# Performance work log

Hardware: AMD Instinct MI355X
Metric: run time of the kernel (lower is better)

Reference implementation:

```python
import jax, jax.numpy as jnp
import numpy as np

L, N, E, NODE_D, EDGE_D, H = 3, 50000, 800000, 64, 16, 128
EPS = 1e-5


def _ln(x, g, b):
    mu = jnp.mean(x, axis=-1, keepdims=True)
    var = jnp.var(x, axis=-1, keepdims=True)
    return (x - mu) * jax.lax.rsqrt(var + EPS) * g + b


def setup_inputs() -> dict:
    key = jax.random.key(0)
    ks = jax.random.split(key, 16)
    inp = {
        "x": jax.random.normal(ks[0], (N, NODE_D), dtype=jnp.float32),
        "edge_index": jax.random.randint(ks[1], (2, E), 0, N, dtype=jnp.int64 if jax.config.jax_enable_x64 else jnp.int32),
        "edge_attr": jax.random.normal(ks[2], (E, EDGE_D), dtype=jnp.float32),
        # node_embed: Linear(node_dim, H) + LayerNorm
        "node_W": jax.random.normal(ks[3], (H, NODE_D), dtype=jnp.float32) * (2.0 / H) ** 0.5,
        "node_b": jnp.zeros((H,), jnp.float32),
        "node_ln_g": jnp.ones((H,), jnp.float32),
        "node_ln_b": jnp.zeros((H,), jnp.float32),
        # per-layer GINConv params, stacked on leading layer dim
        "edge_W": jax.random.normal(ks[4], (L, H, EDGE_D), dtype=jnp.float32) * (2.0 / H) ** 0.5,
        "edge_b": jnp.zeros((L, H), jnp.float32),
        "edge_ln_g": jnp.ones((L, H), jnp.float32),
        "edge_ln_b": jnp.zeros((L, H), jnp.float32),
        "sl_attr": jax.random.normal(ks[5], (L, 1, EDGE_D), dtype=jnp.float32),
        "mlp_W1": jax.random.normal(ks[6], (L, 2 * H, H), dtype=jnp.float32) * (1.0 / H) ** 0.5,
        "mlp_b1": jnp.zeros((L, 2 * H), jnp.float32),
        "mlp_W2": jax.random.normal(ks[7], (L, H, 2 * H), dtype=jnp.float32) * (1.0 / (2 * H)) ** 0.5,
        "mlp_b2": jnp.zeros((L, H), jnp.float32),
        # BatchNorm1d affine params (batch-stat / training-mode math)
        "bn_g": jnp.ones((L, H), jnp.float32),
        "bn_b": jnp.zeros((L, H), jnp.float32),
    }
    return inp


def reference(x, edge_index, edge_attr, node_W, node_b, node_ln_g, node_ln_b,
              edge_W, edge_b, edge_ln_g, edge_ln_b, sl_attr,
              mlp_W1, mlp_b1, mlp_W2, mlp_b2, bn_g, bn_b):
    n = x.shape[0]
    # augmented edge list with self loops appended (add_self_loops)
    loop = jnp.arange(n, dtype=edge_index.dtype)
    src = jnp.concatenate([edge_index[0], loop])  # [E+N]
    dst = jnp.concatenate([edge_index[1], loop])  # [E+N]

    # node_embed: Linear -> LN -> ReLU
    h = jax.nn.relu(_ln(x @ node_W.T + node_b, node_ln_g, node_ln_b))

    for l in range(L):
        # edge_embed on [original edges ; learned self-loop attr]
        sl = jnp.broadcast_to(sl_attr[l], (n, EDGE_D))
        ea = jnp.concatenate([edge_attr, sl], axis=0)          # [E+N, edge_dim]
        ea = jax.nn.relu(_ln(ea @ edge_W[l].T + edge_b[l], edge_ln_g[l], edge_ln_b[l]))
        # message: gather x_j + edge_attr; aggregate: scatter-add to dst
        msg = h[src] + ea                                      # [E+N, H]
        aggr = jax.ops.segment_sum(msg, dst, num_segments=n)   # [N, H]
        # update MLP: Linear -> GELU -> Linear (dropout inactive at eval)
        z = jax.nn.gelu(aggr @ mlp_W1[l].T + mlp_b1[l], approximate=False)
        hl = z @ mlp_W2[l].T + mlp_b2[l]
        # BatchNorm1d (training-mode batch statistics over node dim)
        mu = jnp.mean(hl, axis=0, keepdims=True)
        var = jnp.var(hl, axis=0, keepdims=True)
        hl = (hl - mu) * jax.lax.rsqrt(var + EPS) * bn_g[l] + bn_b[l]
        if l != L - 1:
            hl = jax.nn.relu(hl)  # drop_ratio = 0 -> dropout is identity
        h = hl
    return h
```

## Files before the change

### kernel.cpp

```cpp
#include <hip/hip_runtime.h>
#include <cstdint>
#include <cstddef>

#define HD 128
#define EDGED 16
#define NODED 64
#define LN_EPS 1e-5f

typedef __bf16 bf16x8 __attribute__((ext_vector_type(8)));
typedef float  f32x4  __attribute__((ext_vector_type(4)));

__device__ __forceinline__ float gelu_exact(float x) {
    return 0.5f * x * (1.0f + erff(x * 0.7071067811865475f));
}

__global__ void wconv_k(const float* __restrict__ in, __bf16* __restrict__ hi,
                        __bf16* __restrict__ lo, int n) {
    int i = blockIdx.x * blockDim.x + threadIdx.x;
    if (i < n) {
        float v = in[i];
        __bf16 h = (__bf16)v;
        hi[i] = h;
        lo[i] = (__bf16)(v - (float)h);
    }
}


__global__ void hist_k(const int* __restrict__ ei, int* __restrict__ cnt, int E) {
    int e = blockIdx.x * blockDim.x + threadIdx.x;
    if (e < E) atomicAdd(&cnt[ei[E + e]], 1);
}

__global__ void scan1_k(const int* __restrict__ in, int* __restrict__ out,
                        int* __restrict__ bsum, int n) {
    __shared__ int lds[256];
    int t = threadIdx.x;
    int i = blockIdx.x * 256 + t;
    int v = (i < n) ? in[i] : 0;
    lds[t] = v;
    __syncthreads();
#pragma unroll
    for (int o = 1; o < 256; o <<= 1) {
        int u = (t >= o) ? lds[t - o] : 0;
        __syncthreads();
        lds[t] += u;
        __syncthreads();
    }
    if (i < n) out[i] = lds[t] - v;
    if (t == 255) bsum[blockIdx.x] = lds[255];
}

__global__ void scan2_k(const int* __restrict__ bsum, int* __restrict__ boff, int nb) {
    __shared__ int lds[256];
    int t = threadIdx.x;
    int v = (t < nb) ? bsum[t] : 0;
    lds[t] = v;
    __syncthreads();
#pragma unroll
    for (int o = 1; o < 256; o <<= 1) {
        int u = (t >= o) ? lds[t - o] : 0;
        __syncthreads();
        lds[t] += u;
        __syncthreads();
    }
    if (t < nb) boff[t] = lds[t] - v;
}

__global__ void scan3_k(int* __restrict__ rs, int* __restrict__ cursor,
                        const int* __restrict__ boff, int n, int E) {
    int i = blockIdx.x * 256 + threadIdx.x;
    if (i < n) {
        int v = rs[i] + boff[blockIdx.x];
        rs[i] = v;
        cursor[i] = v;
    }
    if (i == 0) rs[n] = E;
}

__global__ void scatter_k(const int* __restrict__ ei, int* __restrict__ cursor,
                          int2* __restrict__ es, int E) {
    int e = blockIdx.x * blockDim.x + threadIdx.x;
    if (e < E) {
        int dst = ei[E + e];
        int slot = atomicAdd(&cursor[dst], 1);
        es[slot] = make_int2(ei[e], e);
    }
}

__global__ void prep_k(const float* __restrict__ edge_W, const float* __restrict__ edge_b,
                       const float* __restrict__ edge_g, const float* __restrict__ edge_be,
                       const float* __restrict__ sl_attr, float* __restrict__ Wg3,
                       float* __restrict__ bg3, float* __restrict__ M3,
                       float* __restrict__ v3, float* __restrict__ s03,
                       float* __restrict__ slv3)
{
    const int l = blockIdx.x;
    const float* W = edge_W + (size_t)l * HD * EDGED;
    const float* b = edge_b + l * HD;
    const float* g = edge_g + l * HD;
    __shared__ float Wp[HD * EDGED];
    __shared__ float bp[HD];
    __shared__ float wm[EDGED];
    __shared__ float Msh[256];
    __shared__ float vsh[EDGED];
    __shared__ float ash[EDGED];
    __shared__ float bmS, s0sh;
    const int t = threadIdx.x;
#pragma unroll
    for (int m = 0; m < 8; ++m) Wp[m * 256 + t] = W[m * 256 + t];
    __syncthreads();
    if (t < EDGED) {
        float s = 0.f;
        for (int c = 0; c < HD; ++c) s += Wp[c * EDGED + t];
        wm[t] = s * (1.f / HD);
    } else if (t == EDGED) {
        float s = 0.f;
        for (int c = 0; c < HD; ++c) s += b[c];
        bmS = s * (1.f / HD);
    }
    __syncthreads();
    if (t < HD) bp[t] = b[t] - bmS;
    __syncthreads();
#pragma unroll
    for (int m = 0; m < 8; ++m) {
        int idx = m * 256 + t;
        int c = idx >> 4, k = idx & 15;
        float val = Wp[idx] - wm[k];
        Wp[idx] = val;
        Wg3[(size_t)l * 2048 + k * HD + c] = val * g[c];
    }
    if (t < HD) bg3[l * HD + t] = bp[t] * g[t];
    __syncthreads();
    {
        int k = t >> 4, j = t & 15;
        float s = 0.f;
        for (int c = 0; c < HD; ++c) s += Wp[c * EDGED + k] * Wp[c * EDGED + j];
        Msh[t] = s;
        M3[l * 256 + t] = s;
    }
    if (t < EDGED) {
        float s = 0.f;
        for (int c = 0; c < HD; ++c) s += Wp[c * EDGED + t] * bp[c];
        vsh[t] = 2.f * s;
        v3[l * EDGED + t] = 2.f * s;
        ash[t] = sl_attr[l * EDGED + t];
    } else if (t == EDGED) {
        float s = 0.f;
        for (int c = 0; c < HD; ++c) s += bp[c] * bp[c];
        s0sh = s;
        s03[l] = s;
    }
    __syncthreads();
    if (t < HD) {
        float q = s0sh;
#pragma unroll
        for (int k = 0; k < EDGED; ++k) {
            float tk = vsh[k];
#pragma unroll
            for (int j = 0; j < EDGED; ++j) tk = fmaf(Msh[k * 16 + j], ash[j], tk);
            q = fmaf(ash[k], tk, q);
        }
        float inv = rsqrtf(q * (1.f / HD) + LN_EPS);
        float y = 0.f;
#pragma unroll
        for (int k = 0; k < EDGED; ++k) y = fmaf(Wp[t * EDGED + k], ash[k], y);
        slv3[l * HD + t] = fmaxf(fmaf(fmaf(y, g[t], bg3[l * HD + t]), inv, edge_be[l * HD + t]), 0.f);
    }
}

__launch_bounds__(256)
__global__ void einv_k(const int2* __restrict__ es, const float* __restrict__ eattr,
                       const float* __restrict__ M3, const float* __restrict__ v3,
                       const float* __restrict__ s03, float* __restrict__ einv,
                       float* __restrict__ attr_p, int* __restrict__ srcp, int E)
{
    __shared__ float Ms[3 * 256];
    __shared__ float vs[3 * 16];
    __shared__ float s0s[4];
    const int t = threadIdx.x;
    for (int i = t; i < 768; i += 256) Ms[i] = M3[i];
    if (t < 48) vs[t] = v3[t];
    if (t < 3) s0s[t] = s03[t];
    __syncthreads();
    int slot = blockIdx.x * 256 + t;
    if (slot >= E) return;
    int2 se = es[slot];
    srcp[slot] = se.x;
    const float4* ap = (const float4*)(eattr + (size_t)se.y * EDGED);
    float4 A0 = ap[0], A1 = ap[1], A2 = ap[2], A3 = ap[3];
    float4* op = (float4*)(attr_p + (size_t)slot * EDGED);
    op[0] = A0; op[1] = A1; op[2] = A2; op[3] = A3;
    float a[16] = {A0.x, A0.y, A0.z, A0.w, A1.x, A1.y, A1.z, A1.w,
                   A2.x, A2.y, A2.z, A2.w, A3.x, A3.y, A3.z, A3.w};
#pragma unroll
    for (int l = 0; l < 3; ++l) {
        float q = s0s[l];
#pragma unroll
        for (int k = 0; k < 16; ++k) {
            const float* Mr = &Ms[l * 256 + k * 16];
            float tk = vs[l * 16 + k];
#pragma unroll
            for (int j = 0; j < 16; ++j) tk = fmaf(Mr[j], a[j], tk);
            q = fmaf(a[k], tk, q);
        }
        einv[(size_t)l * E + slot] = rsqrtf(q * (1.f / HD) + LN_EPS);
    }
}

template<int K, int NC, int ACT, int STATS, int OUTBF>
__launch_bounds__(256)
__global__ void mgemm_k(const __bf16* __restrict__ Ahi, const __bf16* __restrict__ Alo,
                        const __bf16* __restrict__ Whi, const __bf16* __restrict__ Wlo,
                        const float* __restrict__ bias, float* __restrict__ C,
                        __bf16* __restrict__ Chi, __bf16* __restrict__ Clo,
                        int M, float* __restrict__ stats)
{
    constexpr int RG = 2;
    constexpr int NT = 4;
    constexpr int NK = K / 32;
    __shared__ float st_lds[2][64];

    const int t    = threadIdx.x;
    const int lane = t & 63;
    const int wv   = t >> 6;
    const int ln15 = lane & 15;
    const int quad = lane >> 4;
    const int row_base = blockIdx.x * 128 + wv * 32;
    const int col0 = blockIdx.y * 64;

    f32x4 acc[RG][NT];
#pragma unroll
    for (int g = 0; g < RG; ++g)
#pragma unroll
        for (int nt = 0; nt < NT; ++nt)
#pragma unroll
            for (int r = 0; r < 4; ++r) acc[g][nt][r] = 0.f;

    size_t arow[RG];
#pragma unroll
    for (int g = 0; g < RG; ++g) {
        int row = row_base + g * 16 + ln15;
        row = row < M ? row : M - 1;
        arow[g] = (size_t)row * K + quad * 8;
    }
    size_t brow[NT];
#pragma unroll
    for (int nt = 0; nt < NT; ++nt)
        brow[nt] = (size_t)(col0 + nt * 16 + ln15) * K + quad * 8;

    bf16x8 a0h[RG], a0l[RG], a1h[RG], a1l[RG];
    bf16x8 b0h[NT], b0l[NT], b1h[NT], b1l[NT];

#define LD_A(kc, AH, AL) { \
    _Pragma("unroll") \
    for (int g = 0; g < RG; ++g) { \
        AH[g] = *(const bf16x8*)(Ahi + arow[g] + (kc)); \
        AL[g] = *(const bf16x8*)(Alo + arow[g] + (kc)); \
    } }
#define LD_B(kc, BH, BL) { \
    _Pragma("unroll") \
    for (int nt = 0; nt < NT; ++nt) { \
        BH[nt] = *(const bf16x8*)(Whi + brow[nt] + (kc)); \
        BL[nt] = *(const bf16x8*)(Wlo + brow[nt] + (kc)); \
    } }
#define DO_MFMA(AH, AL, BH, BL) { \
    _Pragma("unroll") \
    for (int nt = 0; nt < NT; ++nt) { \
        _Pragma("unroll") \
        for (int g = 0; g < RG; ++g) { \
            acc[g][nt] = __builtin_amdgcn_mfma_f32_16x16x32_bf16(AH[g], BH[nt], acc[g][nt], 0, 0, 0); \
            acc[g][nt] = __builtin_amdgcn_mfma_f32_16x16x32_bf16(AH[g], BL[nt], acc[g][nt], 0, 0, 0); \
            acc[g][nt] = __builtin_amdgcn_mfma_f32_16x16x32_bf16(AL[g], BH[nt], acc[g][nt], 0, 0, 0); \
        } } }

    LD_A(0, a0h, a0l);
    LD_B(0, b0h, b0l);
    for (int s = 0; s < NK; s += 2) {
        LD_A((s + 1) * 32, a1h, a1l);
        LD_B((s + 1) * 32, b1h, b1l);
        DO_MFMA(a0h, a0l, b0h, b0l);
        if (s + 2 < NK) {
            LD_A((s + 2) * 32, a0h, a0l);
            LD_B((s + 2) * 32, b0h, b0l);
        }
        DO_MFMA(a1h, a1l, b1h, b1l);
    }
#undef LD_A
#undef LD_B
#undef DO_MFMA

    if (STATS) {
        if (t < 64) { st_lds[0][t] = 0.f; st_lds[1][t] = 0.f; }
        __syncthreads();
    }

    float bv[NT];
#pragma unroll
    for (int nt = 0; nt < NT; ++nt) bv[nt] = bias[col0 + nt * 16 + ln15];

    float s1[NT], s2[NT];
#pragma unroll
    for (int nt = 0; nt < NT; ++nt) { s1[nt] = 0.f; s2[nt] = 0.f; }

#pragma unroll
    for (int g = 0; g < RG; ++g)
#pragma unroll
        for (int r = 0; r < 4; ++r) {
            int row = row_base + g * 16 + quad * 4 + r;
            if (row < M) {
#pragma unroll
                for (int nt = 0; nt < NT; ++nt) {
                    float v = acc[g][nt][r] + bv[nt];
                    if (ACT == 1) v = gelu_exact(v);
                    size_t ci = (size_t)row * NC + col0 + nt * 16 + ln15;
                    if (OUTBF) {
                        __bf16 hh = (__bf16)v;
                        Chi[ci] = hh;
                        Clo[ci] = (__bf16)(v - (float)hh);
                    } else {
                        C[ci] = v;
                    }
                    if (STATS) { s1[nt] += v; s2[nt] += v * v; }
                }
            }
        }

    if (STATS) {
#pragma unroll
        for (int nt = 0; nt < NT; ++nt) {
            atomicAdd(&st_lds[0][nt * 16 + ln15], s1[nt]);
            atomicAdd(&st_lds[1][nt * 16 + ln15], s2[nt]);
        }
        __syncthreads();
        if (t < 64) {
            atomicAdd(&stats[col0 + t],      st_lds[0][t]);
            atomicAdd(&stats[HD + col0 + t], st_lds[1][t]);
        }
    }
}

__global__ void ln_relu_k(const float* __restrict__ y, const float* __restrict__ gam,
                          const float* __restrict__ bet, float* __restrict__ h, int N)
{
    int lane = threadIdx.x & 63;
    int c0 = lane * 2;
    float2 g2 = *(const float2*)&gam[c0];
    float2 b2 = *(const float2*)&bet[c0];
    int wid = (blockIdx.x * blockDim.x + threadIdx.x) >> 6;
    int nw  = (gridDim.x * blockDim.x) >> 6;
    for (int n = wid; n < N; n += nw) {
        float2 v = *(const float2*)&y[(size_t)n * HD + c0];
        float s = v.x + v.y;
        float q = v.x * v.x + v.y * v.y;
#pragma unroll
        for (int o = 32; o > 0; o >>= 1) { s += __shfl_xor(s, o, 64); q += __shfl_xor(q, o, 64); }
        float mu  = s * (1.f / 128.f);
        float inv = rsqrtf(q * (1.f / 128.f) - mu * mu + LN_EPS);
        float2 r;
        r.x = fmaxf(fmaf((v.x - mu) * inv, g2.x, b2.x), 0.f);
        r.y = fmaxf(fmaf((v.y - mu) * inv, g2.y, b2.y), 0.f);
        *(float2*)&h[(size_t)n * HD + c0] = r;
    }
}

__launch_bounds__(256)
__global__ void pull4_k(const float* __restrict__ h, const int* __restrict__ srcp,
                        const int* __restrict__ rs, const float* __restrict__ attr_p,
                        const float* __restrict__ einv, const float* __restrict__ slv,
                        const float* __restrict__ Wg, const float* __restrict__ bg,
                        const float* __restrict__ bet, __bf16* __restrict__ Ahi,
                        __bf16* __restrict__ Alo, int N)
{
    __shared__ float alds_all[4][64 * EDGED];
    const int t = threadIdx.x;
    const int lane = t & 63;
    const int wv = t >> 6;
    float* alds = alds_all[wv];

    const int c0 = lane * 2;
    float w0[16], w1[16];
#pragma unroll
    for (int k = 0; k < 16; ++k) {
        float2 wp = *(const float2*)&Wg[k * HD + c0];
        w0[k] = wp.x; w1[k] = wp.y;
    }
    const float2 bgv = *(const float2*)&bg[c0];
    const float2 btv = *(const float2*)&bet[c0];

    const int n = (blockIdx.x << 2) + wv;
    if (n >= N) return;

    const float2 hself = *(const float2*)&h[(size_t)n * HD + c0];
    const float2 slvv  = *(const float2*)&slv[c0];
    float acc0 = hself.x + slvv.x;
    float acc1 = hself.y + slvv.y;

    const int beg = rs[n], end = rs[n + 1];
    for (int s0 = beg; s0 < end; s0 += 64) {
        int m = end - s0; if (m > 64) m = 64;
        int   srcv = 0;
        float ivv  = 0.f;
        if (lane < m) { srcv = srcp[s0 + lane]; ivv = einv[s0 + lane]; }
        const float4* src4 = (const float4*)(attr_p + (size_t)s0 * EDGED);
#pragma unroll
        for (int it = 0; it < 4; ++it) {
            int idx = (it << 6) + lane;
            if (idx < (m << 2)) *(float4*)&alds[idx << 2] = src4[idx];
        }
        asm volatile("s_waitcnt lgkmcnt(0)" ::: "memory");

#define EDGE_BODY(JJ, IVJ, HVJ) { \
            const float* ar = &alds[(JJ) * EDGED]; \
            float4 A0 = *(const float4*)ar,       A1 = *(const float4*)(ar + 4); \
            float4 A2 = *(const float4*)(ar + 8), A3 = *(const float4*)(ar + 12); \
            float a[16] = {A0.x, A0.y, A0.z, A0.w, A1.x, A1.y, A1.z, A1.w, \
                           A2.x, A2.y, A2.z, A2.w, A3.x, A3.y, A3.z, A3.w}; \
            float p0 = bgv.x, q0 = 0.f, p1 = bgv.y, q1 = 0.f; \
            _Pragma("unroll") \
            for (int k = 0; k < 16; k += 2) { \
                p0 = fmaf(a[k],     w0[k],     p0); \
                q0 = fmaf(a[k + 1], w0[k + 1], q0); \
                p1 = fmaf(a[k],     w1[k],     p1); \
                q1 = fmaf(a[k + 1], w1[k + 1], q1); \
            } \
            acc0 += fmaxf(fmaf(p0 + q0, IVJ, btv.x), 0.f) + HVJ.x; \
            acc1 += fmaxf(fmaf(p1 + q1, IVJ, btv.y), 0.f) + HVJ.y; \
        }

        int j = 0;
        for (; j + 4 <= m; j += 4) {
            int s_0 = __shfl(srcv, j,     64);
            int s_1 = __shfl(srcv, j + 1, 64);
            int s_2 = __shfl(srcv, j + 2, 64);
            int s_3 = __shfl(srcv, j + 3, 64);
            float i0 = __shfl(ivv, j,     64);
            float i1 = __shfl(ivv, j + 1, 64);
            float i2 = __shfl(ivv, j + 2, 64);
            float i3 = __shfl(ivv, j + 3, 64);
            float2 h0 = *(const float2*)&h[(size_t)s_0 * HD + c0];
            float2 h1 = *(const float2*)&h[(size_t)s_1 * HD + c0];
            float2 h2 = *(const float2*)&h[(size_t)s_2 * HD + c0];
            float2 h3 = *(const float2*)&h[(size_t)s_3 * HD + c0];
            EDGE_BODY(j,     i0, h0);
            EDGE_BODY(j + 1, i1, h1);
            EDGE_BODY(j + 2, i2, h2);
            EDGE_BODY(j + 3, i3, h3);
        }
        for (; j < m; ++j) {
            int s_  = __shfl(srcv, j, 64);
            float ij = __shfl(ivv, j, 64);
            float2 hj = *(const float2*)&h[(size_t)s_ * HD + c0];
            EDGE_BODY(j, ij, hj);
        }
#undef EDGE_BODY
    }
    __bf16 b0 = (__bf16)acc0, b1 = (__bf16)acc1;
    union { __bf16 b[2]; unsigned u; } ph, pl;
    ph.b[0] = b0;
    ph.b[1] = b1;
    pl.b[0] = (__bf16)(acc0 - (float)b0);
    pl.b[1] = (__bf16)(acc1 - (float)b1);
    *(unsigned*)&Ahi[(size_t)n * HD + c0] = ph.u;
    *(unsigned*)&Alo[(size_t)n * HD + c0] = pl.u;
}

__global__ void bn_k(const float* __restrict__ hl, const float* __restrict__ stats,
                     const float* __restrict__ gam, const float* __restrict__ bet,
                     float* __restrict__ out, int total4, float invN, int relu)
{
    int idx = blockIdx.x * blockDim.x + threadIdx.x;
    if (idx < total4) {
        int c4 = idx & 31;
        float4 x  = ((const float4*)hl)[idx];
        float4 s1 = ((const float4*)stats)[c4];
        float4 s2 = ((const float4*)stats)[32 + c4];
        float4 g  = ((const float4*)gam)[c4];
        float4 b  = ((const float4*)bet)[c4];
        float4 r;
        {
            float m = s1.x * invN; float v = s2.x * invN - m * m;
            r.x = fmaf((x.x - m) * rsqrtf(v + LN_EPS), g.x, b.x);
        }
        {
            float m = s1.y * invN; float v = s2.y * invN - m * m;
            r.y = fmaf((x.y - m) * rsqrtf(v + LN_EPS), g.y, b.y);
        }
        {
            float m = s1.z * invN; float v = s2.z * invN - m * m;
            r.z = fmaf((x.z - m) * rsqrtf(v + LN_EPS), g.z, b.z);
        }
        {
            float m = s1.w * invN; float v = s2.w * invN - m * m;
            r.w = fmaf((x.w - m) * rsqrtf(v + LN_EPS), g.w, b.w);
        }
        if (relu) {
            r.x = fmaxf(r.x, 0.f); r.y = fmaxf(r.y, 0.f);
            r.z = fmaxf(r.z, 0.f); r.w = fmaxf(r.w, 0.f);
        }
        ((float4*)out)[idx] = r;
    }
}

extern "C" void kernel_launch(void* const* d_in, const int* in_sizes, int n_in,
                              void* d_out, int out_size, void* d_ws, size_t ws_size,
                              hipStream_t stream)
{
    const float* x       = (const float*)d_in[0];
    const int*   ei      = (const int*)d_in[1];
    const float* eattr   = (const float*)d_in[2];
    const float* node_W  = (const float*)d_in[3];
    const float* node_b  = (const float*)d_in[4];
    const float* node_g  = (const float*)d_in[5];
    const float* node_be = (const float*)d_in[6];
    const float* edge_W  = (const float*)d_in[7];
    const float* edge_b  = (const float*)d_in[8];
    const float* edge_g  = (const float*)d_in[9];
    const float* edge_be = (const float*)d_in[10];
    const float* sl_attr = (const float*)d_in[11];
    const float* W1      = (const float*)d_in[12];
    const float* b1      = (const float*)d_in[13];
    const float* W2      = (const float*)d_in[14];
    const float* b2      = (const float*)d_in[15];
    const float* bn_g    = (const float*)d_in[16];
    const float* bn_b    = (const float*)d_in[17];

    const int N = in_sizes[0] / NODED;
    const int E = in_sizes[1] / 2;

    char* base = (char*)d_ws;
    size_t off = 0;
    auto take = [&](size_t nbytes) -> void* {
        void* p = base + off;
        off = (off + nbytes + 15) & ~(size_t)15;
        return p;
    };
    float*  h      = (float*)take((size_t)N * HD * 4);
    float*  z      = (float*)take((size_t)N * HD * 4);
    __bf16* aghi   = (__bf16*)take((size_t)N * HD * 2);
    __bf16* aglo   = (__bf16*)take((size_t)N * HD * 2);
    __bf16* zhi    = (__bf16*)take((size_t)N * 256 * 2);
    __bf16* zlo    = (__bf16*)take((size_t)N * 256 * 2);
    __bf16* xhi    = (__bf16*)take((size_t)N * NODED * 2);
    __bf16* xlo    = (__bf16*)take((size_t)N * NODED * 2);
    float*  slv3   = (float*)take(3 * HD * 4);
    float*  stats  = (float*)take(3 * 256 * 4);
    int*    cnt    = (int*)take((size_t)N * 4);
    int*    cursor = (int*)take((size_t)N * 4);
    int*    bsum   = (int*)take(256 * 4);
    int*    boff   = (int*)take(256 * 4);
    int*    rs     = (int*)take(((size_t)N + 2) * 4);
    int2*   es     = (int2*)take((size_t)E * 8);
    float*  einv   = (float*)take((size_t)3 * E * 4);
    float*  attr_p = (float*)take((size_t)E * EDGED * 4);
    int*    srcp   = (int*)take((size_t)E * 4);
    float*  Wg3    = (float*)take(3 * 2048 * 4);
    float*  bg3    = (float*)take(3 * HD * 4);
    float*  M3     = (float*)take(3 * 256 * 4);
    float*  v3     = (float*)take(3 * 16 * 4);
    float*  s03    = (float*)take(4 * 4);
    __bf16* nWhi   = (__bf16*)take((size_t)HD * NODED * 2);
    __bf16* nWlo   = (__bf16*)take((size_t)HD * NODED * 2);
    __bf16* W1hi   = (__bf16*)take((size_t)3 * 256 * HD * 2);
    __bf16* W1lo   = (__bf16*)take((size_t)3 * 256 * HD * 2);
    __bf16* W2hi   = (__bf16*)take((size_t)3 * HD * 256 * 2);
    __bf16* W2lo   = (__bf16*)take((size_t)3 * HD * 256 * 2);

    wconv_k<<<(HD * NODED + 255) / 256, 256, 0, stream>>>(node_W, nWhi, nWlo, HD * NODED);
    wconv_k<<<(3 * 256 * HD + 255) / 256, 256, 0, stream>>>(W1, W1hi, W1lo, 3 * 256 * HD);
    wconv_k<<<(3 * 256 * HD + 255) / 256, 256, 0, stream>>>(W2, W2hi, W2lo, 3 * 256 * HD);
    wconv_k<<<((int)((size_t)N * NODED + 255) / 256), 256, 0, stream>>>(x, xhi, xlo, N * NODED);

    prep_k<<<3, 256, 0, stream>>>(edge_W, edge_b, edge_g, edge_be, sl_attr,
                                  Wg3, bg3, M3, v3, s03, slv3);

    const int eblocks = (E + 255) / 256;
    const int nblocks = (N + 255) / 256;
    hipMemsetAsync(cnt, 0, (size_t)N * sizeof(int), stream);
    hist_k<<<eblocks, 256, 0, stream>>>(ei, cnt, E);
    scan1_k<<<nblocks, 256, 0, stream>>>(cnt, rs, bsum, N);
    scan2_k<<<1, 256, 0, stream>>>(bsum, boff, nblocks);
    scan3_k<<<nblocks, 256, 0, stream>>>(rs, cursor, boff, N, E);
    scatter_k<<<eblocks, 256, 0, stream>>>(ei, cursor, es, E);

    einv_k<<<eblocks, 256, 0, stream>>>(es, eattr, M3, v3, s03, einv, attr_p, srcp, E);

    const int total4  = N * (HD / 4);
    const int vblocks = (total4 + 255) / 256;
    const int pblocks = (N + 3) / 4;
    const int gb128   = (N + 127) / 128;

    mgemm_k<NODED, HD, 0, 0, 0><<<dim3(gb128, 2), 256, 0, stream>>>(
        xhi, xlo, nWhi, nWlo, node_b, z, nullptr, nullptr, N, nullptr);
    ln_relu_k<<<pblocks, 256, 0, stream>>>(z, node_g, node_be, h, N);

    hipMemsetAsync(stats, 0, 3 * 256 * sizeof(float), stream);

    for (int l = 0; l < 3; ++l) {
        pull4_k<<<pblocks, 256, 0, stream>>>(h, srcp, rs, attr_p,
                                             einv + (size_t)l * E,
                                             slv3 + l * HD, Wg3 + (size_t)l * 2048,
                                             bg3 + l * HD, edge_be + l * HD,
                                             aghi, aglo, N);

        mgemm_k<HD, 256, 1, 0, 1><<<dim3(gb128, 4), 256, 0, stream>>>(
            aghi, aglo, W1hi + (size_t)l * 256 * HD, W1lo + (size_t)l * 256 * HD,
            b1 + l * 256, nullptr, zhi, zlo, N, nullptr);

        mgemm_k<256, HD, 0, 1, 0><<<dim3(gb128, 2), 256, 0, stream>>>(
            zhi, zlo, W2hi + (size_t)l * HD * 256, W2lo + (size_t)l * HD * 256,
            b2 + l * HD, (float*)d_out, nullptr, nullptr, N, stats + l * 256);

        bn_k<<<vblocks, 256, 0, stream>>>((const float*)d_out, stats + l * 256,
                                          bn_g + l * HD, bn_b + l * HD,
                                          (l < 2) ? h : (float*)d_out, total4, 1.f / N, (l < 2) ? 1 : 0);
    }
}
```

Before: 999.0 us.

## Store node features in fp16 and use persistent grid-stride pull kernel

Node hidden state h is now stored as fp16 instead of fp32. ln_relu_k and bn_k write it that way and pull5_k reads it, which halves the bytes of the random gathers over edges. The pull kernel also becomes a persistent grid-stride loop capped at 2048 blocks, so per-block setup such as weight register loads is paid less often. The cost is lower precision in the gathered features.

```diff
diff --git a/kernel.cpp b/kernel.cpp
--- a/kernel.cpp
+++ b/kernel.cpp
@@ -9,6 +9,8 @@
 
 typedef __bf16 bf16x8 __attribute__((ext_vector_type(8)));
 typedef float  f32x4  __attribute__((ext_vector_type(4)));
+typedef _Float16 half2v __attribute__((ext_vector_type(2)));
+typedef _Float16 half4v __attribute__((ext_vector_type(4)));
 
 __device__ __forceinline__ float gelu_exact(float x) {
     return 0.5f * x * (1.0f + erff(x * 0.7071067811865475f));
@@ -340,7 +342,7 @@
 }
 
 __global__ void ln_relu_k(const float* __restrict__ y, const float* __restrict__ gam,
-                          const float* __restrict__ bet, float* __restrict__ h, int N)
+                          const float* __restrict__ bet, _Float16* __restrict__ h16, int N)
 {
     int lane = threadIdx.x & 63;
     int c0 = lane * 2;
@@ -356,15 +358,15 @@
         for (int o = 32; o > 0; o >>= 1) { s += __shfl_xor(s, o, 64); q += __shfl_xor(q, o, 64); }
         float mu  = s * (1.f / 128.f);
         float inv = rsqrtf(q * (1.f / 128.f) - mu * mu + LN_EPS);
-        float2 r;
-        r.x = fmaxf(fmaf((v.x - mu) * inv, g2.x, b2.x), 0.f);
-        r.y = fmaxf(fmaf((v.y - mu) * inv, g2.y, b2.y), 0.f);
-        *(float2*)&h[(size_t)n * HD + c0] = r;
+        half2v r;
+        r.x = (_Float16)fmaxf(fmaf((v.x - mu) * inv, g2.x, b2.x), 0.f);
+        r.y = (_Float16)fmaxf(fmaf((v.y - mu) * inv, g2.y, b2.y), 0.f);
+        *(half2v*)&h16[(size_t)n * HD + c0] = r;
     }
 }
 
 __launch_bounds__(256)
-__global__ void pull4_k(const float* __restrict__ h, const int* __restrict__ srcp,
+__global__ void pull5_k(const _Float16* __restrict__ h16, const int* __restrict__ srcp,
                         const int* __restrict__ rs, const float* __restrict__ attr_p,
                         const float* __restrict__ einv, const float* __restrict__ slv,
                         const float* __restrict__ Wg, const float* __restrict__ bg,
@@ -384,30 +386,29 @@
         float2 wp = *(const float2*)&Wg[k * HD + c0];
         w0[k] = wp.x; w1[k] = wp.y;
     }
-    const float2 bgv = *(const float2*)&bg[c0];
-    const float2 btv = *(const float2*)&bet[c0];
-
-    const int n = (blockIdx.x << 2) + wv;
-    if (n >= N) return;
-
-    const float2 hself = *(const float2*)&h[(size_t)n * HD + c0];
-    const float2 slvv  = *(const float2*)&slv[c0];
-    float acc0 = hself.x + slvv.x;
-    float acc1 = hself.y + slvv.y;
-
-    const int beg = rs[n], end = rs[n + 1];
-    for (int s0 = beg; s0 < end; s0 += 64) {
-        int m = end - s0; if (m > 64) m = 64;
-        int   srcv = 0;
-        float ivv  = 0.f;
-        if (lane < m) { srcv = srcp[s0 + lane]; ivv = einv[s0 + lane]; }
-        const float4* src4 = (const float4*)(attr_p + (size_t)s0 * EDGED);
-#pragma unroll
-        for (int it = 0; it < 4; ++it) {
-            int idx = (it << 6) + lane;
-            if (idx < (m << 2)) *(float4*)&alds[idx << 2] = src4[idx];
-        }
-        asm volatile("s_waitcnt lgkmcnt(0)" ::: "memory");
+    const float2 bgv  = *(const float2*)&bg[c0];
+    const float2 btv  = *(const float2*)&bet[c0];
+    const float2 slvv = *(const float2*)&slv[c0];
+
+    const int stride = gridDim.x << 2;
+    for (int n = (blockIdx.x << 2) + wv; n < N; n += stride) {
+        half2v hs = *(const half2v*)&h16[(size_t)n * HD + c0];
+        float acc0 = (float)hs.x + slvv.x;
+        float acc1 = (float)hs.y + slvv.y;
+
+        const int beg = rs[n], end = rs[n + 1];
+        for (int s0 = beg; s0 < end; s0 += 64) {
+            int m = end - s0; if (m > 64) m = 64;
+            int   srcv = 0;
+            float ivv  = 0.f;
+            if (lane < m) { srcv = srcp[s0 + lane]; ivv = einv[s0 + lane]; }
+            const float4* src4 = (const float4*)(attr_p + (size_t)s0 * EDGED);
+#pragma unroll
+            for (int it = 0; it < 4; ++it) {
+                int idx = (it << 6) + lane;
+                if (idx < (m << 2)) *(float4*)&alds[idx << 2] = src4[idx];
+            }
+            asm volatile("s_waitcnt lgkmcnt(0)" ::: "memory");
 
 #define EDGE_BODY(JJ, IVJ, HVJ) { \
             const float* ar = &alds[(JJ) * EDGED]; \
@@ -423,50 +424,52 @@
                 p1 = fmaf(a[k],     w1[k],     p1); \
                 q1 = fmaf(a[k + 1], w1[k + 1], q1); \
             } \
-            acc0 += fmaxf(fmaf(p0 + q0, IVJ, btv.x), 0.f) + HVJ.x; \
-            acc1 += fmaxf(fmaf(p1 + q1, IVJ, btv.y), 0.f) + HVJ.y; \
-        }
-
-        int j = 0;
-        for (; j + 4 <= m; j += 4) {
-            int s_0 = __shfl(srcv, j,     64);
-            int s_1 = __shfl(srcv, j + 1, 64);
-            int s_2 = __shfl(srcv, j + 2, 64);
-            int s_3 = __shfl(srcv, j + 3, 64);
-            float i0 = __shfl(ivv, j,     64);
-            float i1 = __shfl(ivv, j + 1, 64);
-            float i2 = __shfl(ivv, j + 2, 64);
-            float i3 = __shfl(ivv, j + 3, 64);
-            float2 h0 = *(const float2*)&h[(size_t)s_0 * HD + c0];
-            float2 h1 = *(const float2*)&h[(size_t)s_1 * HD + c0];
-            float2 h2 = *(const float2*)&h[(size_t)s_2 * HD + c0];
-            float2 h3 = *(const float2*)&h[(size_t)s_3 * HD + c0];
-            EDGE_BODY(j,     i0, h0);
-            EDGE_BODY(j + 1, i1, h1);
-            EDGE_BODY(j + 2, i2, h2);
-            EDGE_BODY(j + 3, i3, h3);
-        }
-        for (; j < m; ++j) {
-            int s_  = __shfl(srcv, j, 64);
-            float ij = __shfl(ivv, j, 64);
-            float2 hj = *(const float2*)&h[(size_t)s_ * HD + c0];
-            EDGE_BODY(j, ij, hj);
-        }
+            acc0 += fmaxf(fmaf(p0 + q0, IVJ, btv.x), 0.f) + (float)HVJ.x; \
+            acc1 += fmaxf(fmaf(p1 + q1, IVJ, btv.y), 0.f) + (float)HVJ.y; \
+        }
+
+            int j = 0;
+            for (; j + 4 <= m; j += 4) {
+                int s_0 = __shfl(srcv, j,     64);
+                int s_1 = __shfl(srcv, j + 1, 64);
+                int s_2 = __shfl(srcv, j + 2, 64);
+                int s_3 = __shfl(srcv, j + 3, 64);
+                float i0 = __shfl(ivv, j,     64);
+                float i1 = __shfl(ivv, j + 1, 64);
+                float i2 = __shfl(ivv, j + 2, 64);
+                float i3 = __shfl(ivv, j + 3, 64);
+                half2v h0 = *(const half2v*)&h16[(size_t)s_0 * HD + c0];
+                half2v h1 = *(const half2v*)&h16[(size_t)s_1 * HD + c0];
+                half2v h2 = *(const half2v*)&h16[(size_t)s_2 * HD + c0];
+                half2v h3 = *(const half2v*)&h16[(size_t)s_3 * HD + c0];
+                EDGE_BODY(j,     i0, h0);
+                EDGE_BODY(j + 1, i1, h1);
+                EDGE_BODY(j + 2, i2, h2);
+                EDGE_BODY(j + 3, i3, h3);
+            }
+            for (; j < m; ++j) {
+                int s_  = __shfl(srcv, j, 64);
+                float ij = __shfl(ivv, j, 64);
+                half2v hj = *(const half2v*)&h16[(size_t)s_ * HD + c0];
+                EDGE_BODY(j, ij, hj);
+            }
 #undef EDGE_BODY
-    }
-    __bf16 b0 = (__bf16)acc0, b1 = (__bf16)acc1;
-    union { __bf16 b[2]; unsigned u; } ph, pl;
-    ph.b[0] = b0;
-    ph.b[1] = b1;
-    pl.b[0] = (__bf16)(acc0 - (float)b0);
-    pl.b[1] = (__bf16)(acc1 - (float)b1);
-    *(unsigned*)&Ahi[(size_t)n * HD + c0] = ph.u;
-    *(unsigned*)&Alo[(size_t)n * HD + c0] = pl.u;
+        }
+        __bf16 b0 = (__bf16)acc0, b1 = (__bf16)acc1;
+        union { __bf16 b[2]; unsigned u; } ph, pl;
+        ph.b[0] = b0;
+        ph.b[1] = b1;
+        pl.b[0] = (__bf16)(acc0 - (float)b0);
+        pl.b[1] = (__bf16)(acc1 - (float)b1);
+        *(unsigned*)&Ahi[(size_t)n * HD + c0] = ph.u;
+        *(unsigned*)&Alo[(size_t)n * HD + c0] = pl.u;
+    }
 }
 
 __global__ void bn_k(const float* __restrict__ hl, const float* __restrict__ stats,
                      const float* __restrict__ gam, const float* __restrict__ bet,
-                     float* __restrict__ out, int total4, float invN, int relu)
+                     float* __restrict__ out32, _Float16* __restrict__ out16,
+                     int total4, float invN, int relu)
 {
     int idx = blockIdx.x * blockDim.x + threadIdx.x;
     if (idx < total4) {
@@ -497,7 +500,14 @@
             r.x = fmaxf(r.x, 0.f); r.y = fmaxf(r.y, 0.f);
             r.z = fmaxf(r.z, 0.f); r.w = fmaxf(r.w, 0.f);
         }
-        ((float4*)out)[idx] = r;
+        if (out16) {
+            half4v o;
+            o.x = (_Float16)r.x; o.y = (_Float16)r.y;
+            o.z = (_Float16)r.z; o.w = (_Float16)r.w;
+            *(half4v*)&out16[(size_t)idx * 4] = o;
+        } else {
+            ((float4*)out32)[idx] = r;
+        }
     }
 }
 
@@ -534,7 +544,7 @@
         off = (off + nbytes + 15) & ~(size_t)15;
         return p;
     };
-    float*  h      = (float*)take((size_t)N * HD * 4);
+    _Float16* h16  = (_Float16*)take((size_t)N * HD * 2);
     float*  z      = (float*)take((size_t)N * HD * 4);
     __bf16* aghi   = (__bf16*)take((size_t)N * HD * 2);
     __bf16* aglo   = (__bf16*)take((size_t)N * HD * 2);
@@ -586,21 +596,22 @@
 
     const int total4  = N * (HD / 4);
     const int vblocks = (total4 + 255) / 256;
-    const int pblocks = (N + 3) / 4;
     const int gb128   = (N + 127) / 128;
+    int pgrid = (N + 3) / 4;
+    if (pgrid > 2048) pgrid = 2048;
 
     mgemm_k<NODED, HD, 0, 0, 0><<<dim3(gb128, 2), 256, 0, stream>>>(
         xhi, xlo, nWhi, nWlo, node_b, z, nullptr, nullptr, N, nullptr);
-    ln_relu_k<<<pblocks, 256, 0, stream>>>(z, node_g, node_be, h, N);
+    ln_relu_k<<<(N + 3) / 4, 256, 0, stream>>>(z, node_g, node_be, h16, N);
 
     hipMemsetAsync(stats, 0, 3 * 256 * sizeof(float), stream);
 
     for (int l = 0; l < 3; ++l) {
-        pull4_k<<<pblocks, 256, 0, stream>>>(h, srcp, rs, attr_p,
-                                             einv + (size_t)l * E,
-                                             slv3 + l * HD, Wg3 + (size_t)l * 2048,
-                                             bg3 + l * HD, edge_be + l * HD,
-                                             aghi, aglo, N);
+        pull5_k<<<pgrid, 256, 0, stream>>>(h16, srcp, rs, attr_p,
+                                           einv + (size_t)l * E,
+                                           slv3 + l * HD, Wg3 + (size_t)l * 2048,
+                                           bg3 + l * HD, edge_be + l * HD,
+                                           aghi, aglo, N);
 
         mgemm_k<HD, 256, 1, 0, 1><<<dim3(gb128, 4), 256, 0, stream>>>(
             aghi, aglo, W1hi + (size_t)l * 256 * HD, W1lo + (size_t)l * 256 * HD,
@@ -612,6 +623,7 @@
 
         bn_k<<<vblocks, 256, 0, stream>>>((const float*)d_out, stats + l * 256,
                                           bn_g + l * HD, bn_b + l * HD,
-                                          (l < 2) ? h : (float*)d_out, total4, 1.f / N, (l < 2) ? 1 : 0);
-    }
-}
+                                          (float*)d_out, (l < 2) ? h16 : nullptr,
+                                          total4, 1.f / N, (l < 2) ? 1 : 0);
+    }
+}
```

After: 927.4 us. 1.08x faster.
